# Performance work log

Hardware: AMD Instinct MI355X
Metric: run time of the kernel (lower is better)

Reference implementation:

```python
import jax, jax.numpy as jnp
import numpy as np

SR = 48000.0
STAB_EPS = 1e-3
BS = 32
N_FRAMES = 128
N_SAMPLES = 65536


def setup_inputs() -> dict:
    key = jax.random.key(0)
    ks = jax.random.split(key, 8)
    f0_hz = jax.random.uniform(ks[0], (BS,), minval=50.0, maxval=500.0)
    note_on_duration = jax.random.uniform(ks[1], (BS,), minval=0.3, maxval=1.0)
    phase = jax.random.uniform(ks[2], (BS,), minval=-np.pi, maxval=np.pi)
    logits = jax.random.normal(ks[3], (BS, N_FRAMES, 5))
    osc_shape = jax.random.uniform(ks[4], (BS,))
    osc_gain = jax.random.uniform(ks[5], (BS,), minval=0.5, maxval=1.0)
    dist_gain = jax.random.uniform(ks[6], (BS,), minval=1.0, maxval=4.0)
    learned_alpha = jax.random.uniform(ks[7], (BS,), minval=0.5, maxval=3.0)
    return dict(f0_hz=f0_hz, note_on_duration=note_on_duration, phase=phase,
                logits=logits, osc_shape=osc_shape, osc_gain=osc_gain,
                dist_gain=dist_gain, learned_alpha=learned_alpha,
                n_samples=N_SAMPLES)


def lin_interp_dim1(x, n_out):
    """Linear interpolation along dim 1 with align_corners=True. x: (bs, n_in, c)."""
    n_in = x.shape[1]
    pos = jnp.linspace(0.0, n_in - 1.0, n_out)
    i0 = jnp.floor(pos).astype(jnp.int32)
    i1 = jnp.minimum(i0 + 1, n_in - 1)
    frac = (pos - i0.astype(x.dtype))[None, :, None]
    return x[:, i0] * (1.0 - frac) + x[:, i1] * frac


def square_saw_vco(f0_hz, osc_shape, n_samples, phase):
    """torchsynth-style square/saw morph oscillator. f0_hz, osc_shape, phase: (bs,)."""
    f0 = f0_hz[:, None]                                   # (bs, 1)
    inc = jnp.broadcast_to(f0 / SR, (f0.shape[0], n_samples))
    arg = 2.0 * jnp.pi * jnp.cumsum(inc, axis=1) + phase[:, None]
    partials = 12000.0 / (f0 * jnp.log10(f0))
    square = jnp.tanh(jnp.pi * partials * jnp.sin(arg) / 2.0)
    s = osc_shape[:, None]
    return (1.0 - s / 2.0) * square * (1.0 + s * jnp.cos(arg / 2.0))


def exp_decay_env(alpha, note_on_duration, n_samples):
    t = jnp.arange(n_samples, dtype=jnp.float32) / SR     # (n,)
    ramp = jnp.clip(1.0 - t[None, :] / note_on_duration[:, None], STAB_EPS, 1.0)
    env = ramp ** alpha[:, None]
    return jnp.where(t[None, :] <= note_on_duration[:, None], env, 0.0)


def logits_to_a_coeff_triangle(a_logits):
    """Map 2 logits to a stable biquad denominator (a1, a2) inside the stability triangle."""
    stab = 1.0 - STAB_EPS
    a1 = 2.0 * jnp.tanh(a_logits[..., 0]) * stab
    a1_abs = jnp.abs(a1)
    a2 = ((2.0 - a1_abs) * jnp.tanh(a_logits[..., 1]) * stab + a1_abs) / 2.0
    return jnp.stack([a1, a2], axis=-1)


def sample_wise_lpc(x, a):
    """Time-varying all-pole order-2: y[t] = x[t] - a1[t]*y[t-1] - a2[t]*y[t-2].
    x: (bs, n), a: (bs, n, 2). Sequential lax.scan over time."""
    def step(carry, inp):
        y1, y2 = carry
        xt, a1, a2 = inp
        y = xt - a1 * y1 - a2 * y2
        return (y, y1), y
    z = jnp.zeros(x.shape[0], dtype=x.dtype)
    xs = (x.T, a[..., 0].T, a[..., 1].T)                  # time-major
    _, ys = jax.lax.scan(step, (z, z), xs)
    return ys.T


def time_varying_fir(x, b):
    """y[t] = b0[t]*x[t] + b1[t]*x[t-1] + b2[t]*x[t-2], zero initial state."""
    x1 = jnp.pad(x, ((0, 0), (1, 0)))[:, :-1]
    x2 = jnp.pad(x, ((0, 0), (2, 0)))[:, :-2]
    return b[..., 0] * x + b[..., 1] * x1 + b[..., 2] * x2


def reference(f0_hz, note_on_duration, phase, logits, osc_shape, osc_gain,
              dist_gain, learned_alpha, n_samples):
    # --- oscillator + envelope ---
    dry = square_saw_vco(f0_hz, osc_shape, n_samples, phase)
    dry = dry * osc_gain[:, None]
    envelope = exp_decay_env(learned_alpha, note_on_duration, n_samples)
    dry = dry * envelope
    # --- coefficients (interp_logits=False: map to coeffs at frame rate, then upsample) ---
    a_coeff = logits_to_a_coeff_triangle(logits[..., :2])   # (bs, n_frames, 2)
    b_coeff = logits[..., 2:]                                # (bs, n_frames, 3)
    a_coeff = lin_interp_dim1(a_coeff, n_samples)            # (bs, n, 2)
    b_coeff = lin_interp_dim1(b_coeff, n_samples)            # (bs, n, 3)
    # --- time-varying biquad: all-pole recursion then FIR ---
    y_a = sample_wise_lpc(dry, a_coeff)
    y_ab = time_varying_fir(y_a, b_coeff)
    # --- distortion ---
    wet = jnp.tanh(y_ab * dist_gain[:, None])
    a0 = jnp.ones_like(a_coeff[:, :, 0])
    a_coeff3 = jnp.stack([a0, a_coeff[:, :, 0], a_coeff[:, :, 1]], axis=2)
    return (dry, wet, envelope, y_ab, a_coeff3, b_coeff, y_a)
```

## Files before the change

### kernel.cpp

```cpp
#include <hip/hip_runtime.h>
#include <cmath>

#define DI __device__ __forceinline__

constexpr int BS = 32;
constexpr int NS = 65536;
constexpr int NF = 128;
constexpr int S  = 4;
constexpr int TB = 256;
constexpr int SAMP = TB * S;
constexpr int NC = NS / SAMP;
constexpr size_t U = (size_t)BS * NS;
constexpr double PI_D = 3.14159265358979323846;
constexpr float STAB = 0.999f;

typedef float f4 __attribute__((ext_vector_type(4)));
DI f4 mkf4(float a, float b, float c, float d) { f4 r; r.x=a; r.y=b; r.z=c; r.w=d; return r; }
DI void ntst4(const f4 v, float* p) { __builtin_nontemporal_store(v, (f4*)p); }

struct M6 { float a, b, c, d, u, v; };

DI M6 comp(const M6& R, const M6& L) {
    M6 o;
    o.a = fmaf(R.a, L.a, R.b * L.c);
    o.b = fmaf(R.a, L.b, R.b * L.d);
    o.c = fmaf(R.c, L.a, R.d * L.c);
    o.d = fmaf(R.c, L.b, R.d * L.d);
    o.u = fmaf(R.a, L.u, fmaf(R.b, L.v, R.u));
    o.v = fmaf(R.c, L.u, fmaf(R.d, L.v, R.v));
    return o;
}

DI void stepL(M6& A, float a1, float a2, float x) {
    float na = fmaf(-a1, A.a, -a2 * A.c);
    float nb = fmaf(-a1, A.b, -a2 * A.d);
    float nu = fmaf(-a1, A.u, fmaf(-a2, A.v, x));
    A.c = A.a; A.d = A.b; A.v = A.u;
    A.a = na;  A.b = nb;  A.u = nu;
}

template<int CTRL> DI float dppf(float x) {
    return __int_as_float(__builtin_amdgcn_update_dpp(
        __float_as_int(x), __float_as_int(x), CTRL, 0xF, 0xF, false));
}
template<int CTRL> DI M6 dpp6(const M6& s) {
    M6 o;
    o.a = dppf<CTRL>(s.a); o.b = dppf<CTRL>(s.b);
    o.c = dppf<CTRL>(s.c); o.d = dppf<CTRL>(s.d);
    o.u = dppf<CTRL>(s.u); o.v = dppf<CTRL>(s.v);
    return o;
}
DI void sel6(M6& s, const M6& t, bool p) {
    s.a = p ? t.a : s.a; s.b = p ? t.b : s.b; s.c = p ? t.c : s.c;
    s.d = p ? t.d : s.d; s.u = p ? t.u : s.u; s.v = p ? t.v : s.v;
}
DI void wave_scan6(M6& s, int lane) {
    const int sub = lane & 15;
    { M6 o = dpp6<0x111>(s); M6 t = comp(s, o); sel6(s, t, sub >= 1); }
    { M6 o = dpp6<0x112>(s); M6 t = comp(s, o); sel6(s, t, sub >= 2); }
    { M6 o = dpp6<0x114>(s); M6 t = comp(s, o); sel6(s, t, sub >= 4); }
    { M6 o = dpp6<0x118>(s); M6 t = comp(s, o); sel6(s, t, sub >= 8); }
    { M6 o = dpp6<0x142>(s); M6 t = comp(s, o); sel6(s, t, (lane & 16) != 0); }
    { M6 o = dpp6<0x143>(s); M6 t = comp(s, o); sel6(s, t, lane >= 32); }
}

DI M6 ld6(const float* p) { M6 m; m.a=p[0]; m.b=p[1]; m.c=p[2]; m.d=p[3]; m.u=p[4]; m.v=p[5]; return m; }
DI void st6(float* p, const M6& m) { p[0]=m.a; p[1]=m.b; p[2]=m.c; p[3]=m.d; p[4]=m.u; p[5]=m.v; }

DI void ipos(int t, int& i0, int& i1, float& fr) {
    int pn = t * 127;
    int p0 = pn / 65535;
    i0 = p0;
    i1 = (p0 + 1 > 127) ? 127 : p0 + 1;
    fr = (float)(pn - p0 * 65535) * (1.0f / 65535.0f);
}

DI float fast_tanh(float x) {
    float e = __expf(2.0f * x);
    return 1.0f - 2.0f / (e + 1.0f);
}

DI void stage_frames(const float* __restrict__ logits, int b, int F, int tid,
                     float (*sfa)[2], float (*sfb)[3]) {
    if (tid < 4) {
        int fidx = F + tid; if (fidx > 127) fidx = 127;
        const float* L = logits + (size_t)(b * NF + fidx) * 5;
        float a1 = 2.0f * tanhf(L[0]) * STAB;
        float aa = fabsf(a1);
        float a2 = ((2.0f - aa) * tanhf(L[1]) * STAB + aa) * 0.5f;
        sfa[tid][0] = a1; sfa[tid][1] = a2;
        sfb[tid][0] = L[2]; sfb[tid][1] = L[3]; sfb[tid][2] = L[4];
    }
}

DI void interp4(int t0, int F, const float (*sfa)[2], const float (*sfb)[3],
                float* a1v, float* a2v, float* b0v, float* b1v, float* b2v) {
    #pragma unroll
    for (int k = 0; k < S; k++) {
        int i0, i1; float fr;
        ipos(t0 + k, i0, i1, fr);
        float w0 = 1.0f - fr;
        int l0 = i0 - F, l1 = i1 - F;
        a1v[k] = sfa[l0][0] * w0 + sfa[l1][0] * fr;
        a2v[k] = sfa[l0][1] * w0 + sfa[l1][1] * fr;
        b0v[k] = sfb[l0][0] * w0 + sfb[l1][0] * fr;
        b1v[k] = sfb[l0][1] * w0 + sfb[l1][1] * fr;
        b2v[k] = sfb[l0][2] * w0 + sfb[l1][2] * fr;
    }
}

DI void osc4(int t0, float f0, float ph, float sh, float gn, float dur, float al,
             float* x, float* env4) {
    const double inc = (double)f0 / 48000.0;
    const float partials = 12000.0f / (f0 * __log10f(f0));
    const double cum0 = (double)(t0 + 1) * inc;
    const double uu0 = cum0 - 2.0 * floor(cum0 * 0.5);
    const float theta0 = (float)(PI_D * uu0 + 0.5 * (double)ph);
    const float dth = (float)(PI_D * inc);
    #pragma unroll
    for (int k = 0; k < S; k++) {
        int t = t0 + k;
        float theta = theta0 + (float)k * dth;
        float sn, cs;
        __sincosf(theta, &sn, &cs);
        float sq = fast_tanh(1.57079632679f * partials * (2.0f * sn * cs));
        float dry0 = (1.0f - 0.5f * sh) * sq * (1.0f + sh * cs);
        float tsec = (float)t * (1.0f / 48000.0f);
        float env = 0.0f;
        if (tsec <= dur) {
            float ramp = 1.0f - tsec / dur;
            ramp = ramp < 0.001f ? 0.001f : (ramp > 1.0f ? 1.0f : ramp);
            env = __expf(al * __logf(ramp));
        }
        env4[k] = env;
        x[k] = dry0 * gn * env;
    }
}

__global__ __launch_bounds__(TB) void k_osc(
    const float* __restrict__ f0_hz, const float* __restrict__ note_dur,
    const float* __restrict__ phase, const float* __restrict__ logits,
    const float* __restrict__ osc_shape, const float* __restrict__ osc_gain,
    const float* __restrict__ alpha,
    float* __restrict__ ws_chunk, float* __restrict__ out) {
    __shared__ float sfa[4][2], sfb[4][3], wt[4][6];
    __shared__ float sstage[SAMP * 3];
    const int bid = blockIdx.x;
    const int b = bid / NC, c = bid % NC;
    const int tid = threadIdx.x;
    const int t0 = c * SAMP + tid * S;
    const size_t g0 = (size_t)b * NS + t0;
    const int F = (c * SAMP * 127) / 65535;

    stage_frames(logits, b, F, tid, sfa, sfb);

    float x[S], env4[S];
    osc4(t0, f0_hz[b], phase[b], osc_shape[b], osc_gain[b], note_dur[b], alpha[b],
         x, env4);
    __syncthreads();

    float a1v[S], a2v[S], b0v[S], b1v[S], b2v[S];
    interp4(t0, F, sfa, sfb, a1v, a2v, b0v, b1v, b2v);

    ntst4(mkf4(x[0], x[1], x[2], x[3]), &out[g0]);
    ntst4(mkf4(env4[0], env4[1], env4[2], env4[3]), &out[2 * U + g0]);

    const int tw = tid * 12;
    const size_t blk0 = ((size_t)b * NS + (size_t)c * SAMP) * 3;
    *(f4*)&sstage[tw + 0] = mkf4(1.0f, a1v[0], a2v[0], 1.0f);
    *(f4*)&sstage[tw + 4] = mkf4(a1v[1], a2v[1], 1.0f, a1v[2]);
    *(f4*)&sstage[tw + 8] = mkf4(a2v[2], 1.0f, a1v[3], a2v[3]);
    __syncthreads();
    {
        float* dst = out + 4 * U + blk0;
        #pragma unroll
        for (int r = 0; r < 3; r++) {
            int wi = r * (TB * 4) + tid * 4;
            ntst4(*(const f4*)&sstage[wi], &dst[wi]);
        }
    }
    __syncthreads();
    *(f4*)&sstage[tw + 0] = mkf4(b0v[0], b1v[0], b2v[0], b0v[1]);
    *(f4*)&sstage[tw + 4] = mkf4(b1v[1], b2v[1], b0v[2], b1v[2]);
    *(f4*)&sstage[tw + 8] = mkf4(b2v[2], b0v[3], b1v[3], b2v[3]);
    __syncthreads();
    {
        float* dst = out + 7 * U + blk0;
        #pragma unroll
        for (int r = 0; r < 3; r++) {
            int wi = r * (TB * 4) + tid * 4;
            ntst4(*(const f4*)&sstage[wi], &dst[wi]);
        }
    }

    M6 A; A.a = -a1v[0]; A.b = -a2v[0]; A.c = 1.0f; A.d = 0.0f; A.u = x[0]; A.v = 0.0f;
    #pragma unroll
    for (int k = 1; k < S; k++) stepL(A, a1v[k], a2v[k], x[k]);

    const int lane = tid & 63, w = tid >> 6;
    wave_scan6(A, lane);
    if (lane == 63) st6(wt[w], A);
    __syncthreads();
    if (tid == TB - 1) {
        M6 p = ld6(wt[0]);
        p = comp(ld6(wt[1]), p);
        p = comp(ld6(wt[2]), p);
        M6 tot = comp(A, p);
        st6(ws_chunk + ((size_t)b * NC + c) * 6, tot);
    }
}

__global__ __launch_bounds__(TB) void k_iir(
    const float* __restrict__ f0_hz, const float* __restrict__ note_dur,
    const float* __restrict__ phase, const float* __restrict__ logits,
    const float* __restrict__ osc_shape, const float* __restrict__ osc_gain,
    const float* __restrict__ dist_gain, const float* __restrict__ alpha,
    const float* __restrict__ ws_chunk, float* __restrict__ out) {
    __shared__ float sfa[4][2], sfb[4][3], wt[4][6], sv[NC][2];
    const int bid = blockIdx.x;
    const int b = bid / NC, c = bid % NC;
    const int tid = threadIdx.x;
    const int t0 = c * SAMP + tid * S;
    const size_t g0 = (size_t)b * NS + t0;
    const int F = (c * SAMP * 127) / 65535;

    stage_frames(logits, b, F, tid, sfa, sfb);

    if (tid < NC) {
        M6 cs = ld6(ws_chunk + ((size_t)b * NC + tid) * 6);
        wave_scan6(cs, tid);
        sv[tid][0] = cs.u; sv[tid][1] = cs.v;
    }

    float x[S], env4[S];
    osc4(t0, f0_hz[b], phase[b], osc_shape[b], osc_gain[b], note_dur[b], alpha[b],
         x, env4);

    __syncthreads();
    const float s0 = c ? sv[c - 1][0] : 0.0f;
    const float s1 = c ? sv[c - 1][1] : 0.0f;

    float a1v[S], a2v[S], b0v[S], b1v[S], b2v[S];
    interp4(t0, F, sfa, sfb, a1v, a2v, b0v, b1v, b2v);

    M6 A; A.a = -a1v[0]; A.b = -a2v[0]; A.c = 1.0f; A.d = 0.0f; A.u = x[0]; A.v = 0.0f;
    #pragma unroll
    for (int k = 1; k < S; k++) stepL(A, a1v[k], a2v[k], x[k]);

    const int lane = tid & 63, w = tid >> 6;
    wave_scan6(A, lane);
    if (lane == 63) st6(wt[w], A);
    __syncthreads();

    M6 P; P.a = 1.f; P.b = 0.f; P.c = 0.f; P.d = 1.f; P.u = 0.f; P.v = 0.f;
    for (int i = 0; i < w; i++) P = comp(ld6(wt[i]), P);
    M6 prev;
    prev.a = __shfl_up(A.a, 1, 64); prev.b = __shfl_up(A.b, 1, 64);
    prev.c = __shfl_up(A.c, 1, 64); prev.d = __shfl_up(A.d, 1, 64);
    prev.u = __shfl_up(A.u, 1, 64); prev.v = __shfl_up(A.v, 1, 64);
    M6 E = (lane == 0) ? P : comp(prev, P);

    float y1 = fmaf(E.a, s0, fmaf(E.b, s1, E.u));
    float y2 = fmaf(E.c, s0, fmaf(E.d, s1, E.v));
    const float ys0 = y1, ys1 = y2;

    float y[S];
    #pragma unroll
    for (int k = 0; k < S; k++) {
        y[k] = fmaf(-a1v[k], y1, fmaf(-a2v[k], y2, x[k]));
        y2 = y1; y1 = y[k];
    }

    const float dg = dist_gain[b];
    float yab[S], wet[S];
    #pragma unroll
    for (int k = 0; k < S; k++) {
        float ym1 = (k >= 1) ? y[k - 1] : ys0;
        float ym2 = (k >= 2) ? y[k - 2] : ((k == 1) ? ys0 : ys1);
        yab[k] = b0v[k] * y[k] + b1v[k] * ym1 + b2v[k] * ym2;
        wet[k] = fast_tanh(yab[k] * dg);
    }

    ntst4(mkf4(wet[0], wet[1], wet[2], wet[3]), &out[U + g0]);
    ntst4(mkf4(yab[0], yab[1], yab[2], yab[3]), &out[3 * U + g0]);
    ntst4(mkf4(y[0], y[1], y[2], y[3]), &out[10 * U + g0]);
}

extern "C" void kernel_launch(void* const* d_in, const int* in_sizes, int n_in,
                              void* d_out, int out_size, void* d_ws, size_t ws_size,
                              hipStream_t stream) {
    const float* f0   = (const float*)d_in[0];
    const float* dur  = (const float*)d_in[1];
    const float* ph   = (const float*)d_in[2];
    const float* lg   = (const float*)d_in[3];
    const float* shp  = (const float*)d_in[4];
    const float* gn   = (const float*)d_in[5];
    const float* dist = (const float*)d_in[6];
    const float* alp  = (const float*)d_in[7];
    float* out = (float*)d_out;
    float* ws_chunk = (float*)d_ws;

    k_osc<<<BS * NC, TB, 0, stream>>>(f0, dur, ph, lg, shp, gn, alp, ws_chunk, out);
    k_iir<<<BS * NC, TB, 0, stream>>>(f0, dur, ph, lg, shp, gn, dist, alp, ws_chunk, out);
}
```

Baseline: 129.5 us.

## Fuse oscillator and IIR kernels into one cooperative kernel with grid sync

Merges the two kernels into a single cooperative launch. Each block computes its oscillator samples, coefficients and chunk-level scan transform. It publishes the chunk summary, waits on a grid-wide barrier, then scans the summaries and finishes the recursion with x and the coefficients still in registers. This removes the second launch and the recomputation or reload of the oscillator and coefficients in the IIR pass, at the cost of a grid-wide barrier that needs all 2048 blocks co-resident. If the cooperative launch fails, it falls back to the old two-kernel path.

```diff
diff --git a/kernel.cpp b/kernel.cpp
--- a/kernel.cpp
+++ b/kernel.cpp
@@ -1,5 +1,8 @@
 #include <hip/hip_runtime.h>
+#include <hip/hip_cooperative_groups.h>
 #include <cmath>
+
+namespace cg = cooperative_groups;
 
 #define DI __device__ __forceinline__
 
@@ -137,6 +140,136 @@
     }
 }
 
+__global__ __launch_bounds__(TB, 8) void k_all(
+    const float* __restrict__ f0_hz, const float* __restrict__ note_dur,
+    const float* __restrict__ phase, const float* __restrict__ logits,
+    const float* __restrict__ osc_shape, const float* __restrict__ osc_gain,
+    const float* __restrict__ dist_gain, const float* __restrict__ alpha,
+    float* __restrict__ ws_chunk, float* __restrict__ out) {
+    __shared__ float sfa[4][2], sfb[4][3], wt[4][6], sv[NC][2];
+    __shared__ float sstage[SAMP * 3];
+    const int bid = blockIdx.x;
+    const int b = bid / NC, c = bid % NC;
+    const int tid = threadIdx.x;
+    const int t0 = c * SAMP + tid * S;
+    const size_t g0 = (size_t)b * NS + t0;
+    const int F = (c * SAMP * 127) / 65535;
+
+    stage_frames(logits, b, F, tid, sfa, sfb);
+
+    float x[S], env4[S];
+    osc4(t0, f0_hz[b], phase[b], osc_shape[b], osc_gain[b], note_dur[b], alpha[b],
+         x, env4);
+    __syncthreads();
+
+    float a1v[S], a2v[S], b0v[S], b1v[S], b2v[S];
+    interp4(t0, F, sfa, sfb, a1v, a2v, b0v, b1v, b2v);
+
+    ntst4(mkf4(x[0], x[1], x[2], x[3]), &out[g0]);
+    ntst4(mkf4(env4[0], env4[1], env4[2], env4[3]), &out[2 * U + g0]);
+
+    const int tw = tid * 12;
+    const size_t blk0 = ((size_t)b * NS + (size_t)c * SAMP) * 3;
+    *(f4*)&sstage[tw + 0] = mkf4(1.0f, a1v[0], a2v[0], 1.0f);
+    *(f4*)&sstage[tw + 4] = mkf4(a1v[1], a2v[1], 1.0f, a1v[2]);
+    *(f4*)&sstage[tw + 8] = mkf4(a2v[2], 1.0f, a1v[3], a2v[3]);
+    __syncthreads();
+    {
+        float* dst = out + 4 * U + blk0;
+        #pragma unroll
+        for (int r = 0; r < 3; r++) {
+            int wi = r * (TB * 4) + tid * 4;
+            ntst4(*(const f4*)&sstage[wi], &dst[wi]);
+        }
+    }
+    __syncthreads();
+    *(f4*)&sstage[tw + 0] = mkf4(b0v[0], b1v[0], b2v[0], b0v[1]);
+    *(f4*)&sstage[tw + 4] = mkf4(b1v[1], b2v[1], b0v[2], b1v[2]);
+    *(f4*)&sstage[tw + 8] = mkf4(b2v[2], b0v[3], b1v[3], b2v[3]);
+    __syncthreads();
+    {
+        float* dst = out + 7 * U + blk0;
+        #pragma unroll
+        for (int r = 0; r < 3; r++) {
+            int wi = r * (TB * 4) + tid * 4;
+            ntst4(*(const f4*)&sstage[wi], &dst[wi]);
+        }
+    }
+
+    M6 A; A.a = -a1v[0]; A.b = -a2v[0]; A.c = 1.0f; A.d = 0.0f; A.u = x[0]; A.v = 0.0f;
+    #pragma unroll
+    for (int k = 1; k < S; k++) stepL(A, a1v[k], a2v[k], x[k]);
+
+    const int lane = tid & 63, w = tid >> 6;
+    wave_scan6(A, lane);
+    if (lane == 63) st6(wt[w], A);
+    __syncthreads();
+    if (tid == TB - 1) {
+        M6 p = ld6(wt[0]);
+        p = comp(ld6(wt[1]), p);
+        p = comp(ld6(wt[2]), p);
+        M6 tot = comp(A, p);
+        float* wp = ws_chunk + (size_t)(b * NC + c) * 6;
+        __hip_atomic_store(wp + 0, tot.a, __ATOMIC_RELAXED, __HIP_MEMORY_SCOPE_AGENT);
+        __hip_atomic_store(wp + 1, tot.b, __ATOMIC_RELAXED, __HIP_MEMORY_SCOPE_AGENT);
+        __hip_atomic_store(wp + 2, tot.c, __ATOMIC_RELAXED, __HIP_MEMORY_SCOPE_AGENT);
+        __hip_atomic_store(wp + 3, tot.d, __ATOMIC_RELAXED, __HIP_MEMORY_SCOPE_AGENT);
+        __hip_atomic_store(wp + 4, tot.u, __ATOMIC_RELAXED, __HIP_MEMORY_SCOPE_AGENT);
+        __hip_atomic_store(wp + 5, tot.v, __ATOMIC_RELEASE, __HIP_MEMORY_SCOPE_AGENT);
+    }
+
+    cg::this_grid().sync();
+
+    if (tid < NC) {
+        const float* wp = ws_chunk + (size_t)(b * NC + tid) * 6;
+        M6 cs;
+        cs.v = __hip_atomic_load(wp + 5, __ATOMIC_ACQUIRE, __HIP_MEMORY_SCOPE_AGENT);
+        cs.a = __hip_atomic_load(wp + 0, __ATOMIC_RELAXED, __HIP_MEMORY_SCOPE_AGENT);
+        cs.b = __hip_atomic_load(wp + 1, __ATOMIC_RELAXED, __HIP_MEMORY_SCOPE_AGENT);
+        cs.c = __hip_atomic_load(wp + 2, __ATOMIC_RELAXED, __HIP_MEMORY_SCOPE_AGENT);
+        cs.d = __hip_atomic_load(wp + 3, __ATOMIC_RELAXED, __HIP_MEMORY_SCOPE_AGENT);
+        cs.u = __hip_atomic_load(wp + 4, __ATOMIC_RELAXED, __HIP_MEMORY_SCOPE_AGENT);
+        wave_scan6(cs, tid);
+        sv[tid][0] = cs.u; sv[tid][1] = cs.v;
+    }
+    __syncthreads();
+    const float s0 = c ? sv[c - 1][0] : 0.0f;
+    const float s1 = c ? sv[c - 1][1] : 0.0f;
+
+    M6 P; P.a = 1.f; P.b = 0.f; P.c = 0.f; P.d = 1.f; P.u = 0.f; P.v = 0.f;
+    for (int i = 0; i < w; i++) P = comp(ld6(wt[i]), P);
+    M6 prev;
+    prev.a = __shfl_up(A.a, 1, 64); prev.b = __shfl_up(A.b, 1, 64);
+    prev.c = __shfl_up(A.c, 1, 64); prev.d = __shfl_up(A.d, 1, 64);
+    prev.u = __shfl_up(A.u, 1, 64); prev.v = __shfl_up(A.v, 1, 64);
+    M6 E = (lane == 0) ? P : comp(prev, P);
+
+    float y1 = fmaf(E.a, s0, fmaf(E.b, s1, E.u));
+    float y2 = fmaf(E.c, s0, fmaf(E.d, s1, E.v));
+    const float ys0 = y1, ys1 = y2;
+
+    float y[S];
+    #pragma unroll
+    for (int k = 0; k < S; k++) {
+        y[k] = fmaf(-a1v[k], y1, fmaf(-a2v[k], y2, x[k]));
+        y2 = y1; y1 = y[k];
+    }
+
+    const float dg = dist_gain[b];
+    float yab[S], wet[S];
+    #pragma unroll
+    for (int k = 0; k < S; k++) {
+        float ym1 = (k >= 1) ? y[k - 1] : ys0;
+        float ym2 = (k >= 2) ? y[k - 2] : ((k == 1) ? ys0 : ys1);
+        yab[k] = b0v[k] * y[k] + b1v[k] * ym1 + b2v[k] * ym2;
+        wet[k] = fast_tanh(yab[k] * dg);
+    }
+
+    ntst4(mkf4(wet[0], wet[1], wet[2], wet[3]), &out[U + g0]);
+    ntst4(mkf4(yab[0], yab[1], yab[2], yab[3]), &out[3 * U + g0]);
+    ntst4(mkf4(y[0], y[1], y[2], y[3]), &out[10 * U + g0]);
+}
+
 __global__ __launch_bounds__(TB) void k_osc(
     const float* __restrict__ f0_hz, const float* __restrict__ note_dur,
     const float* __restrict__ phase, const float* __restrict__ logits,
@@ -153,7 +286,6 @@
     const int F = (c * SAMP * 127) / 65535;
 
     stage_frames(logits, b, F, tid, sfa, sfb);
-
     float x[S], env4[S];
     osc4(t0, f0_hz[b], phase[b], osc_shape[b], osc_gain[b], note_dur[b], alpha[b],
          x, env4);
@@ -300,6 +432,14 @@
     float* out = (float*)d_out;
     float* ws_chunk = (float*)d_ws;
 
-    k_osc<<<BS * NC, TB, 0, stream>>>(f0, dur, ph, lg, shp, gn, alp, ws_chunk, out);
-    k_iir<<<BS * NC, TB, 0, stream>>>(f0, dur, ph, lg, shp, gn, dist, alp, ws_chunk, out);
-}
+    void* args[] = {
+        (void*)&f0, (void*)&dur, (void*)&ph, (void*)&lg, (void*)&shp,
+        (void*)&gn, (void*)&dist, (void*)&alp, (void*)&ws_chunk, (void*)&out
+    };
+    hipError_t e = hipLaunchCooperativeKernel((void*)k_all, dim3(BS * NC), dim3(TB),
+                                              args, 0, stream);
+    if (e != hipSuccess) {
+        k_osc<<<BS * NC, TB, 0, stream>>>(f0, dur, ph, lg, shp, gn, alp, ws_chunk, out);
+        k_iir<<<BS * NC, TB, 0, stream>>>(f0, dur, ph, lg, shp, gn, dist, alp, ws_chunk, out);
+    }
+}
```

New measurement: 463.2 us. 258% more time.
